# Performance work log

Measured on AMD Instinct MI355X. Metric: run time of the kernel, lower is better.

The kernel has to match this reference:

```python
import jax, jax.numpy as jnp
import numpy as np


def setup_inputs() -> dict:
    key = jax.random.key(0)
    ks = jax.random.split(key, 4)
    B, S, D, H, E = 2, 2048, 1024, 4096, 8
    scale_in = 1.0 / np.sqrt(D)
    scale_h = 1.0 / np.sqrt(H)
    return {
        "x": jax.random.normal(ks[0], (B, S, D), dtype=jnp.float32),
        "Wr": jax.random.normal(ks[1], (E, D), dtype=jnp.float32) * scale_in,
        "br": jnp.zeros((E,), dtype=jnp.float32),
        "W1": jax.random.normal(ks[2], (E, H, D), dtype=jnp.float32) * scale_in,
        "b1": jnp.zeros((E, H), dtype=jnp.float32),
        "W2": jax.random.normal(ks[3], (E, D, H), dtype=jnp.float32) * scale_h,
        "b2": jnp.zeros((E, D), dtype=jnp.float32),
        "top_k": 2,
    }


def reference(x, Wr, br, W1, b1, W2, b2, top_k):
    B, S, D = x.shape
    E = Wr.shape[0]
    x_flat = x.reshape(-1, D)                                   # [N, D]
    # Router: top-k logits, softmax over the selected k values only
    logits = x_flat @ Wr.T + br                                 # [N, E]
    top_vals, top_idx = jax.lax.top_k(logits, top_k)            # [N, k]
    gates = jax.nn.softmax(top_vals, axis=-1)                   # [N, k]
    # Per-expert combine weight: gate_e[n, e] = sum_k gates[n, k] * 1[top_idx[n,k]==e]
    gate_e = jnp.einsum("nk,nke->ne", gates,
                        jax.nn.one_hot(top_idx, E, dtype=x.dtype))  # [N, E]
    # Dense all-expert MLP (grouped GEMM), then masked combine. Same math as
    # the per-expert gather/scatter loop: unselected experts get zero gate.
    h = jax.nn.relu(jnp.einsum("nd,ehd->neh", x_flat, W1) + b1)     # [N, E, H]
    y = jnp.einsum("neh,edh->ned", h, W2) + b2                      # [N, E, D]
    out = jnp.einsum("ned,ne->nd", y, gate_e)                       # [N, D]
    return out.reshape(B, S, D)
```

## Files before the change

### kernel.cpp

```cpp
#include <hip/hip_runtime.h>
#include <hip/hip_bf16.h>
#include <stdint.h>

#define N_TOK 4096
#define D_ 1024
#define H_ 4096
#define E_ 8
#define NSLOT (N_TOK*2)
#define BM 128
#define BN 128
#define BK 32
#define MAXT 72

typedef __attribute__((ext_vector_type(8))) short short8;
typedef __attribute__((ext_vector_type(4))) float floatx4;
typedef unsigned int u32;

__device__ __forceinline__ unsigned short f2bf(float f){
    union { float f; unsigned int u; } c; c.f = f;
    unsigned int u = c.u;
    unsigned int r = (u + 0x7fffu + ((u >> 16) & 1u)) >> 16;
    return (unsigned short)r;
}

__device__ __forceinline__ void async16(const void* g, void* l){
    __builtin_amdgcn_global_load_lds(
        (const __attribute__((address_space(1))) u32*)g,
        (__attribute__((address_space(3))) u32*)l, 16, 0, 0);
}


__global__ __launch_bounds__(256) void router_kernel(
    const float* __restrict__ x, const float* __restrict__ Wr,
    const float* __restrict__ br, int* __restrict__ topIdx,
    float* __restrict__ topGate)
{
    int n = blockIdx.x * 4 + (threadIdx.x >> 6);
    int lane = threadIdx.x & 63;
    const float4* xp = (const float4*)(x + (size_t)n * D_);
    float acc[E_];
#pragma unroll
    for (int e = 0; e < E_; e++) acc[e] = 0.f;
#pragma unroll
    for (int j = 0; j < 4; j++){
        int idx = j * 64 + lane;
        float4 xv = xp[idx];
#pragma unroll
        for (int e = 0; e < E_; e++){
            float4 wv = ((const float4*)(Wr + (size_t)e * D_))[idx];
            acc[e] += xv.x*wv.x + xv.y*wv.y + xv.z*wv.z + xv.w*wv.w;
        }
    }
#pragma unroll
    for (int e = 0; e < E_; e++){
        float v = acc[e];
        for (int off = 32; off > 0; off >>= 1) v += __shfl_xor(v, off, 64);
        acc[e] = v;
    }
    if (lane == 0){
        float best = -1e30f, second = -1e30f; int bi = 0, si = 0;
#pragma unroll
        for (int e = 0; e < E_; e++){
            float v = acc[e] + br[e];
            if (v > best){ second = best; si = bi; best = v; bi = e; }
            else if (v > second){ second = v; si = e; }
        }
        float e1 = __expf(second - best);
        float denom = 1.f + e1;
        topIdx[n*2+0] = bi;  topIdx[n*2+1] = si;
        topGate[n*2+0] = 1.f/denom;  topGate[n*2+1] = e1/denom;
    }
}

__global__ __launch_bounds__(256) void hist_kernel(
    const int* __restrict__ topIdx, int* __restrict__ hdr)
{
    __shared__ int c[E_];
    int t = threadIdx.x;
    if (t < E_) c[t] = 0;
    __syncthreads();
    int e = topIdx[blockIdx.x * 256 + t];
    atomicAdd(&c[e], 1);
    __syncthreads();
    if (t < E_) hdr[256 + blockIdx.x * E_ + t] = c[t];
}

__global__ __launch_bounds__(64) void scan2_kernel(int* __restrict__ hdr)
{
    __shared__ int cnt[32 * E_];
    __shared__ int tot[E_];
    __shared__ int offs[E_ + 1];
    int t = threadIdx.x;
    for (int i = t; i < 32 * E_; i += 64) cnt[i] = hdr[256 + i];
    __syncthreads();
    if (t < E_){
        int s = 0;
        for (int b = 0; b < 32; b++) s += cnt[b * E_ + t];
        tot[t] = s;
    }
    __syncthreads();
    if (t == 0){
        int o = 0;
        for (int e = 0; e < E_; e++){ offs[e] = o; o += tot[e]; }
        offs[E_] = o;
    }
    __syncthreads();
    if (t < E_ + 1) hdr[16 + t] = offs[t];
    if (t < E_){
        int run = offs[t];
        for (int b = 0; b < 32; b++){ hdr[512 + b * E_ + t] = run; run += cnt[b * E_ + t]; }
    }
    if (t == 0){
        int tn = 0;
        for (int e = 0; e < E_; e++){
            int nt = (tot[e] + BM - 1) >> 7;
            for (int i = 0; i < nt; i++){ hdr[32 + tn] = e; hdr[112 + tn] = offs[e] + (i << 7); tn++; }
        }
        for (; tn < MAXT; tn++){ hdr[32 + tn] = -1; hdr[112 + tn] = 0; }
    }
}

__global__ __launch_bounds__(256) void pos_kernel(
    const int* __restrict__ topIdx, const float* __restrict__ topGate,
    const int* __restrict__ hdr, int* __restrict__ posOf,
    int* __restrict__ rowTok, float* __restrict__ rowGate)
{
    __shared__ int c[E_];
    int t = threadIdx.x;
    if (t < E_) c[t] = 0;
    __syncthreads();
    int slot = blockIdx.x * 256 + t;
    int e = topIdx[slot];
    int r = atomicAdd(&c[e], 1);
    int pos = hdr[512 + blockIdx.x * E_ + e] + r;
    posOf[slot] = pos;
    rowTok[pos] = slot >> 1;
    rowGate[pos] = topGate[slot];
}

__global__ __launch_bounds__(256) void copy_kernel(
    const float* __restrict__ x, const int* __restrict__ posOf,
    unsigned short* __restrict__ xg)
{
    int slot = blockIdx.x * 4 + (threadIdx.x >> 6);
    int lane = threadIdx.x & 63;
    int n = slot >> 1;
    int pos = posOf[slot];
    const float4* xp = (const float4*)(x + (size_t)n * D_);
    ushort4* op = (ushort4*)(xg + (size_t)pos * D_);
#pragma unroll
    for (int j = 0; j < 4; j++){
        float4 v = xp[j * 64 + lane];
        ushort4 o; o.x=f2bf(v.x); o.y=f2bf(v.y); o.z=f2bf(v.z); o.w=f2bf(v.w);
        op[j * 64 + lane] = o;
    }
}

template<int MODE>
__global__ __launch_bounds__(256) void moe_gemm(
    const unsigned short* __restrict__ A, int Ktot,
    const float* __restrict__ Wbase, size_t wStride,
    const float* __restrict__ biasBase, int biasStride,
    const int* __restrict__ hdr,
    const int* __restrict__ rowTok, const float* __restrict__ rowGate,
    unsigned short* __restrict__ hout, float* __restrict__ out)
{
    const int bx = blockIdx.x, by = blockIdx.y;
    int e = hdr[32 + bx];
    if (e < 0) return;
    int rowBase = hdr[112 + bx];
    int validRows = hdr[16 + e + 1] - rowBase;

    __shared__ __align__(16) unsigned short As[BM * BK];
    __shared__ __align__(16) float Bs[BN * BK];

    const float* Wexp  = Wbase + (size_t)e * wStride + (size_t)(by * BN) * Ktot;
    const float* biasE = biasBase + (size_t)e * biasStride + by * BN;

    const int tid  = threadIdx.x;
    const int lane = tid & 63, wave = tid >> 6;
    const int wm = wave & 1, wn = wave >> 1;
    const int l16 = lane & 15, quad = lane >> 4;

    floatx4 acc[4][4];
#pragma unroll
    for (int mi = 0; mi < 4; mi++)
#pragma unroll
        for (int ni = 0; ni < 4; ni++)
            acc[mi][ni] = (floatx4){0.f,0.f,0.f,0.f};

    int aS[2], aRow[2], aCol[2];
#pragma unroll
    for (int i = 0; i < 2; i++){
        int s = wave * 128 + i * 64 + lane;
        aS[i] = s;
        int r = rowBase + (s >> 2);
        aRow[i] = r < (NSLOT - 1) ? r : (NSLOT - 1);
        aCol[i] = (s & 3) * 8;
    }
    int bS[4], bRow[4], bCol[4];
#pragma unroll
    for (int i = 0; i < 4; i++){
        int s = wave * 256 + i * 64 + lane;
        bS[i] = s;
        int r = s >> 3, c = s & 7;
        bRow[i] = r;
        bCol[i] = (c ^ (r & 7)) * 4;
    }

    for (int k0 = 0; k0 < Ktot; k0 += BK){
#pragma unroll
        for (int i = 0; i < 2; i++)
            async16(A + (size_t)aRow[i] * Ktot + k0 + aCol[i], (char*)As + aS[i] * 16);
#pragma unroll
        for (int i = 0; i < 4; i++)
            async16(Wexp + (size_t)bRow[i] * Ktot + k0 + bCol[i], (char*)Bs + bS[i] * 16);
        __syncthreads();

        short8 af[4];
#pragma unroll
        for (int mi = 0; mi < 4; mi++){
            int r = wm * 64 + mi * 16 + l16;
            af[mi] = *(const short8*)(As + r * BK + quad * 8);
        }
        short8 bfr[4];
#pragma unroll
        for (int ni = 0; ni < 4; ni++){
            int n = wn * 64 + ni * 16 + l16;
            int g0 = (2 * quad)     ^ (n & 7);
            int g1 = (2 * quad + 1) ^ (n & 7);
            float4 u0 = *(const float4*)(Bs + n * BK + g0 * 4);
            float4 u1 = *(const float4*)(Bs + n * BK + g1 * 4);
            union { short8 s; __hip_bfloat162 h[4]; } u;
            u.h[0] = __float22bfloat162_rn(make_float2(u0.x, u0.y));
            u.h[1] = __float22bfloat162_rn(make_float2(u0.z, u0.w));
            u.h[2] = __float22bfloat162_rn(make_float2(u1.x, u1.y));
            u.h[3] = __float22bfloat162_rn(make_float2(u1.z, u1.w));
            bfr[ni] = u.s;
        }
#pragma unroll
        for (int mi = 0; mi < 4; mi++)
#pragma unroll
            for (int ni = 0; ni < 4; ni++)
                acc[mi][ni] = __builtin_amdgcn_mfma_f32_16x16x32_bf16(
                    af[mi], bfr[ni], acc[mi][ni], 0, 0, 0);
        __syncthreads();
    }

#pragma unroll
    for (int mi = 0; mi < 4; mi++){
#pragma unroll
        for (int r = 0; r < 4; r++){
            int rl = wm * 64 + mi * 16 + quad * 4 + r;
            if (rl >= validRows) continue;
            int grow = rowBase + rl;
            int   tok  = 0;
            float gate = 0.f;
            if (MODE == 2){ tok = rowTok[grow]; gate = rowGate[grow]; }
#pragma unroll
            for (int ni = 0; ni < 4; ni++){
                int gcol = by * BN + wn * 64 + ni * 16 + l16;
                float v = acc[mi][ni][r] + biasE[wn * 64 + ni * 16 + l16];
                if (MODE == 1){
                    v = v > 0.f ? v : 0.f;
                    hout[(size_t)grow * H_ + gcol] = f2bf(v);
                } else {
                    atomicAdd(out + (size_t)tok * D_ + gcol, gate * v);
                }
            }
        }
    }
}

extern "C" void kernel_launch(void* const* d_in, const int* in_sizes, int n_in,
                              void* d_out, int out_size, void* d_ws, size_t ws_size,
                              hipStream_t stream)
{
    (void)in_sizes; (void)n_in; (void)ws_size;
    const float* x  = (const float*)d_in[0];
    const float* Wr = (const float*)d_in[1];
    const float* br = (const float*)d_in[2];
    const float* W1 = (const float*)d_in[3];
    const float* b1 = (const float*)d_in[4];
    const float* W2 = (const float*)d_in[5];
    const float* b2 = (const float*)d_in[6];
    float* out = (float*)d_out;

    char* ws = (char*)d_ws;
    int*   hdr     = (int*)ws;
    int*   topIdx  = (int*)  (ws + 4096);
    float* topGate = (float*)(ws + 36864);
    int*   posOf   = (int*)  (ws + 69632);
    int*   rowTok  = (int*)  (ws + 102400);
    float* rowGate = (float*)(ws + 135168);
    unsigned short* xg   = (unsigned short*)(ws + 262144);
    unsigned short* hbuf = (unsigned short*)(ws + 17039360);

    hipMemsetAsync(d_out, 0, (size_t)out_size * sizeof(float), stream);

    router_kernel<<<N_TOK/4, 256, 0, stream>>>(x, Wr, br, topIdx, topGate);
    hist_kernel<<<32, 256, 0, stream>>>(topIdx, hdr);
    scan2_kernel<<<1, 64, 0, stream>>>(hdr);
    pos_kernel<<<32, 256, 0, stream>>>(topIdx, topGate, hdr, posOf, rowTok, rowGate);
    copy_kernel<<<NSLOT/4, 256, 0, stream>>>(x, posOf, xg);
    moe_gemm<1><<<dim3(MAXT, H_/BN), 256, 0, stream>>>(
        xg, D_, W1, (size_t)H_ * D_, b1, H_, hdr, rowTok, rowGate, hbuf, nullptr);
    moe_gemm<2><<<dim3(MAXT, D_/BN), 256, 0, stream>>>(
        hbuf, H_, W2, (size_t)D_ * H_, b2, D_, hdr, rowTok, rowGate, nullptr, out);
}
```

Baseline: 649.0 us.

## Pre-convert weights to bf16, use 256x256 double-buffered tiles with split-K

Adds a per-call kernel that converts W1 and W2 to bf16 in workspace. This removes the per-tile fp32 loads and in-LDS conversion, at the cost of an extra pass over all weights on every call. The grouped GEMM moves to 256x256 tiles with 512 threads, a double-buffered async LDS pipeline with manual waitcnt and barriers, an XOR swizzle, and grouped block ordering for L2 reuse. The second GEMM is split four ways along K, with the bias added only by the first split, so more atomic adds hit the output.

Measured after the change: 738.2 us. 1.14x slower.

```diff
diff --git a/kernel.cpp b/kernel.cpp
--- a/kernel.cpp
+++ b/kernel.cpp
@@ -7,10 +7,10 @@
 #define H_ 4096
 #define E_ 8
 #define NSLOT (N_TOK*2)
-#define BM 128
-#define BN 128
+#define BM 256
+#define BN 256
 #define BK 32
-#define MAXT 72
+#define MAXT 40
 
 typedef __attribute__((ext_vector_type(8))) short short8;
 typedef __attribute__((ext_vector_type(4))) float floatx4;
@@ -29,6 +29,25 @@
         (__attribute__((address_space(3))) u32*)l, 16, 0, 0);
 }
 
+__global__ __launch_bounds__(256) void cvt2_kernel(
+    const float* __restrict__ s1, unsigned short* __restrict__ d1, int n1,
+    const float* __restrict__ s2, unsigned short* __restrict__ d2, int n2)
+{
+    int stride = gridDim.x * 256;
+    int tot = n1 + n2;
+    for (int i = blockIdx.x * 256 + threadIdx.x; i < tot; i += stride){
+        if (i < n1){
+            float4 v = ((const float4*)s1)[i];
+            ushort4 o; o.x=f2bf(v.x); o.y=f2bf(v.y); o.z=f2bf(v.z); o.w=f2bf(v.w);
+            ((ushort4*)d1)[i] = o;
+        } else {
+            int j = i - n1;
+            float4 v = ((const float4*)s2)[j];
+            ushort4 o; o.x=f2bf(v.x); o.y=f2bf(v.y); o.z=f2bf(v.z); o.w=f2bf(v.w);
+            ((ushort4*)d2)[j] = o;
+        }
+    }
+}
 
 __global__ __launch_bounds__(256) void router_kernel(
     const float* __restrict__ x, const float* __restrict__ Wr,
@@ -113,8 +132,8 @@
     if (t == 0){
         int tn = 0;
         for (int e = 0; e < E_; e++){
-            int nt = (tot[e] + BM - 1) >> 7;
-            for (int i = 0; i < nt; i++){ hdr[32 + tn] = e; hdr[112 + tn] = offs[e] + (i << 7); tn++; }
+            int nt = (tot[e] + BM - 1) >> 8;
+            for (int i = 0; i < nt; i++){ hdr[32 + tn] = e; hdr[112 + tn] = offs[e] + (i << 8); tn++; }
         }
         for (; tn < MAXT; tn++){ hdr[32 + tn] = -1; hdr[112 + tn] = 0; }
     }
@@ -157,101 +176,112 @@
 }
 
 template<int MODE>
-__global__ __launch_bounds__(256) void moe_gemm(
+__global__ __launch_bounds__(512, 2) void moe_gemm(
     const unsigned short* __restrict__ A, int Ktot,
-    const float* __restrict__ Wbase, size_t wStride,
+    const unsigned short* __restrict__ Wbase, size_t wStride,
     const float* __restrict__ biasBase, int biasStride,
     const int* __restrict__ hdr,
     const int* __restrict__ rowTok, const float* __restrict__ rowGate,
     unsigned short* __restrict__ hout, float* __restrict__ out)
 {
-    const int bx = blockIdx.x, by = blockIdx.y;
+    int gid = blockIdx.y * gridDim.x + blockIdx.x;
+    int groupW = gridDim.y < 8 ? gridDim.y : 8;
+    int per = gridDim.x * groupW;
+    int g = gid / per, rr = gid % per;
+    int by = g * groupW + rr % groupW;
+    int bx = rr / groupW;
+
     int e = hdr[32 + bx];
     if (e < 0) return;
     int rowBase = hdr[112 + bx];
     int validRows = hdr[16 + e + 1] - rowBase;
 
-    __shared__ __align__(16) unsigned short As[BM * BK];
-    __shared__ __align__(16) float Bs[BN * BK];
-
-    const float* Wexp  = Wbase + (size_t)e * wStride + (size_t)(by * BN) * Ktot;
+    int kChunk = Ktot / gridDim.z;
+    int kStart = blockIdx.z * kChunk;
+
+    __shared__ __align__(16) unsigned short As[2][BM * BK];
+    __shared__ __align__(16) unsigned short Bs[2][BN * BK];
+
+    const unsigned short* Wexp = Wbase + (size_t)e * wStride + (size_t)(by * BN) * Ktot;
     const float* biasE = biasBase + (size_t)e * biasStride + by * BN;
 
     const int tid  = threadIdx.x;
     const int lane = tid & 63, wave = tid >> 6;
-    const int wm = wave & 1, wn = wave >> 1;
+    const int wm = wave >> 2, wn = wave & 3;
     const int l16 = lane & 15, quad = lane >> 4;
 
-    floatx4 acc[4][4];
-#pragma unroll
-    for (int mi = 0; mi < 4; mi++)
+    floatx4 acc[8][4];
+#pragma unroll
+    for (int mi = 0; mi < 8; mi++)
 #pragma unroll
         for (int ni = 0; ni < 4; ni++)
             acc[mi][ni] = (floatx4){0.f,0.f,0.f,0.f};
 
-    int aS[2], aRow[2], aCol[2];
+    size_t aOff[2], bOff[2];
+    int    lOff[2];
 #pragma unroll
     for (int i = 0; i < 2; i++){
-        int s = wave * 128 + i * 64 + lane;
-        aS[i] = s;
-        int r = rowBase + (s >> 2);
-        aRow[i] = r < (NSLOT - 1) ? r : (NSLOT - 1);
-        aCol[i] = (s & 3) * 8;
-    }
-    int bS[4], bRow[4], bCol[4];
-#pragma unroll
-    for (int i = 0; i < 4; i++){
-        int s = wave * 256 + i * 64 + lane;
-        bS[i] = s;
-        int r = s >> 3, c = s & 7;
-        bRow[i] = r;
-        bCol[i] = (c ^ (r & 7)) * 4;
-    }
-
-    for (int k0 = 0; k0 < Ktot; k0 += BK){
-#pragma unroll
-        for (int i = 0; i < 2; i++)
-            async16(A + (size_t)aRow[i] * Ktot + k0 + aCol[i], (char*)As + aS[i] * 16);
-#pragma unroll
-        for (int i = 0; i < 4; i++)
-            async16(Wexp + (size_t)bRow[i] * Ktot + k0 + bCol[i], (char*)Bs + bS[i] * 16);
-        __syncthreads();
-
-        short8 af[4];
-#pragma unroll
-        for (int mi = 0; mi < 4; mi++){
-            int r = wm * 64 + mi * 16 + l16;
-            af[mi] = *(const short8*)(As + r * BK + quad * 8);
-        }
-        short8 bfr[4];
+        int s = i * 512 + tid;
+        int r = s >> 2, gst = s & 3;
+        int gsrc = gst ^ ((r >> 1) & 3);
+        int ar = rowBase + r;
+        ar = ar < (NSLOT - 1) ? ar : (NSLOT - 1);
+        aOff[i] = (size_t)ar * Ktot + gsrc * 8;
+        bOff[i] = (size_t)r  * Ktot + gsrc * 8;
+        lOff[i] = s * 16;
+    }
+
+    auto issue = [&](int t, int buf){
+        int kk = kStart + t * BK;
+#pragma unroll
+        for (int i = 0; i < 2; i++){
+            async16(A    + aOff[i] + kk, (char*)As[buf] + lOff[i]);
+            async16(Wexp + bOff[i] + kk, (char*)Bs[buf] + lOff[i]);
+        }
+    };
+
+    int nIter = kChunk / BK;
+    issue(0, 0);
+    issue(1, 1);
+
+    int p = 0;
+    for (int it = 0; it < nIter; it++){
+        if (it < nIter - 1)
+            asm volatile("s_waitcnt vmcnt(4)\ns_barrier" ::: "memory");
+        else
+            asm volatile("s_waitcnt vmcnt(0)\ns_barrier" ::: "memory");
+
+        short8 af[8], bfr[4];
+#pragma unroll
+        for (int mi = 0; mi < 8; mi++){
+            int r = wm * 128 + mi * 16 + l16;
+            int gq = quad ^ ((r >> 1) & 3);
+            af[mi] = *(const short8*)(As[p] + r * BK + gq * 8);
+        }
 #pragma unroll
         for (int ni = 0; ni < 4; ni++){
             int n = wn * 64 + ni * 16 + l16;
-            int g0 = (2 * quad)     ^ (n & 7);
-            int g1 = (2 * quad + 1) ^ (n & 7);
-            float4 u0 = *(const float4*)(Bs + n * BK + g0 * 4);
-            float4 u1 = *(const float4*)(Bs + n * BK + g1 * 4);
-            union { short8 s; __hip_bfloat162 h[4]; } u;
-            u.h[0] = __float22bfloat162_rn(make_float2(u0.x, u0.y));
-            u.h[1] = __float22bfloat162_rn(make_float2(u0.z, u0.w));
-            u.h[2] = __float22bfloat162_rn(make_float2(u1.x, u1.y));
-            u.h[3] = __float22bfloat162_rn(make_float2(u1.z, u1.w));
-            bfr[ni] = u.s;
-        }
-#pragma unroll
-        for (int mi = 0; mi < 4; mi++)
+            int gq = quad ^ ((n >> 1) & 3);
+            bfr[ni] = *(const short8*)(Bs[p] + n * BK + gq * 8);
+        }
+        asm volatile("s_waitcnt lgkmcnt(0)\ns_barrier" ::: "memory");
+        if (it + 2 < nIter) issue(it + 2, p);
+
+#pragma unroll
+        for (int mi = 0; mi < 8; mi++)
 #pragma unroll
             for (int ni = 0; ni < 4; ni++)
                 acc[mi][ni] = __builtin_amdgcn_mfma_f32_16x16x32_bf16(
                     af[mi], bfr[ni], acc[mi][ni], 0, 0, 0);
-        __syncthreads();
-    }
-
-#pragma unroll
-    for (int mi = 0; mi < 4; mi++){
+        p ^= 1;
+    }
+
+    bool addB = (MODE == 1) || (blockIdx.z == 0);
+#pragma unroll
+    for (int mi = 0; mi < 8; mi++){
 #pragma unroll
         for (int r = 0; r < 4; r++){
-            int rl = wm * 64 + mi * 16 + quad * 4 + r;
+            int rl = wm * 128 + mi * 16 + quad * 4 + r;
             if (rl >= validRows) continue;
             int grow = rowBase + rl;
             int   tok  = 0;
@@ -259,8 +289,9 @@
             if (MODE == 2){ tok = rowTok[grow]; gate = rowGate[grow]; }
 #pragma unroll
             for (int ni = 0; ni < 4; ni++){
-                int gcol = by * BN + wn * 64 + ni * 16 + l16;
-                float v = acc[mi][ni][r] + biasE[wn * 64 + ni * 16 + l16];
+                int lcol = wn * 64 + ni * 16 + l16;
+                int gcol = by * BN + lcol;
+                float v = acc[mi][ni][r] + (addB ? biasE[lcol] : 0.f);
                 if (MODE == 1){
                     v = v > 0.f ? v : 0.f;
                     hout[(size_t)grow * H_ + gcol] = f2bf(v);
@@ -295,6 +326,8 @@
     float* rowGate = (float*)(ws + 135168);
     unsigned short* xg   = (unsigned short*)(ws + 262144);
     unsigned short* hbuf = (unsigned short*)(ws + 17039360);
+    unsigned short* w1b  = (unsigned short*)(ws + 84148224);
+    unsigned short* w2b  = (unsigned short*)(ws + 151257088);
 
     hipMemsetAsync(d_out, 0, (size_t)out_size * sizeof(float), stream);
 
@@ -303,8 +336,10 @@
     scan2_kernel<<<1, 64, 0, stream>>>(hdr);
     pos_kernel<<<32, 256, 0, stream>>>(topIdx, topGate, hdr, posOf, rowTok, rowGate);
     copy_kernel<<<NSLOT/4, 256, 0, stream>>>(x, posOf, xg);
-    moe_gemm<1><<<dim3(MAXT, H_/BN), 256, 0, stream>>>(
-        xg, D_, W1, (size_t)H_ * D_, b1, H_, hdr, rowTok, rowGate, hbuf, nullptr);
-    moe_gemm<2><<<dim3(MAXT, D_/BN), 256, 0, stream>>>(
-        hbuf, H_, W2, (size_t)D_ * H_, b2, D_, hdr, rowTok, rowGate, nullptr, out);
-}
+    cvt2_kernel<<<2048, 256, 0, stream>>>(W1, w1b, (E_*H_*D_)/4, W2, w2b, (E_*D_*H_)/4);
+
+    moe_gemm<1><<<dim3(MAXT, H_/BN, 1), 512, 0, stream>>>(
+        xg, D_, w1b, (size_t)H_ * D_, b1, H_, hdr, rowTok, rowGate, hbuf, nullptr);
+    moe_gemm<2><<<dim3(MAXT, D_/BN, 4), 512, 0, stream>>>(
+        hbuf, H_, w2b, (size_t)D_ * H_, b2, D_, hdr, rowTok, rowGate, nullptr, out);
+}
```
